# Performance work log

Measured on AMD Instinct MI355X. Metric: run time of the kernel, lower is better.

Reference implementation:

```python
import jax, jax.numpy as jnp
import numpy as np

C = 1.0          # Poincare ball curvature
EPS = 1e-15      # geoopt-style denominator clamp
ATANH_CLAMP = 1e-7


def _artanh(x):
    x = jnp.clip(x, -1.0 + ATANH_CLAMP, 1.0 - ATANH_CLAMP)
    return 0.5 * (jnp.log1p(x) - jnp.log1p(-x))


def setup_inputs() -> dict:
    key = jax.random.key(0)
    n, d = 8192, 256
    embeddings = jax.random.normal(key, (n, d), dtype=jnp.float32) * 0.01
    return {"embeddings": embeddings}


def reference(embeddings):
    # Pairwise Poincare-ball distance:
    #   dist(x, y) = (2/sqrt(c)) * artanh(sqrt(c) * ||(-x) mobius_add y||)
    # mobius_add(-x, y) = (A*(-x) + B*y) / D with
    #   A = 1 - 2c<x,y> + c||y||^2,  B = 1 - c||x||^2,
    #   D = 1 - 2c<x,y> + c^2 ||x||^2 ||y||^2
    # so ||num||^2 = A^2||x||^2 - 2AB<x,y> + B^2||y||^2, using only Gram-matrix
    # quantities -> avoids the [n,n,d] broadcast the torch code materializes
    # while computing identical math.
    x2 = jnp.sum(embeddings * embeddings, axis=-1)          # [n]
    dot = embeddings @ embeddings.T                          # [n,n]
    xi2 = x2[:, None]                                        # ||x_i||^2
    xj2 = x2[None, :]                                        # ||x_j||^2

    A = 1.0 - 2.0 * C * dot + C * xj2                        # [n,n]
    B = 1.0 - C * xi2                                        # [n,1] broadcast
    D = 1.0 - 2.0 * C * dot + (C * C) * xi2 * xj2            # [n,n]

    num2 = jnp.maximum(A * A * xi2 - 2.0 * A * B * dot + B * B * xj2, 0.0)
    norm = jnp.sqrt(num2) / jnp.maximum(jnp.abs(D), EPS)

    sqrt_c = jnp.sqrt(jnp.asarray(C, embeddings.dtype))
    dists = (2.0 / sqrt_c) * _artanh(sqrt_c * norm)          # [n,n]

    n = embeddings.shape[0]
    probs = jax.nn.sigmoid(-dists) * (1.0 - jnp.eye(n, dtype=dists.dtype))
    return (probs, dists)
```

## Files before the change

### kernel.cpp

```cpp
#include <hip/hip_runtime.h>
#include <hip/hip_bf16.h>
#include <stdint.h>

#define NROW 8192
#define DIM  256
#define TILE 128
#define BK   64

typedef unsigned short u16;
typedef __attribute__((ext_vector_type(8))) short short8;
typedef __attribute__((ext_vector_type(4))) float f32x4;

__device__ __forceinline__ void load_lds16(const void* g, void* l) {
    __builtin_amdgcn_global_load_lds(
        (const __attribute__((address_space(1))) void*)g,
        (__attribute__((address_space(3))) void*)l,
        16, 0, 0);
}

__global__ __launch_bounds__(256) void prep_kernel(const float* __restrict__ emb,
                                                   u16* __restrict__ ebf,
                                                   float* __restrict__ x2) {
    const int row = blockIdx.x;
    const int tid = threadIdx.x;
    float v = emb[(size_t)row * DIM + tid];
    uint32_t bits = __float_as_uint(v);
    uint32_t r = (bits + 0x7FFFu + ((bits >> 16) & 1u)) >> 16;
    ebf[(size_t)row * DIM + tid] = (u16)r;
    float s = v * v;
#pragma unroll
    for (int off = 32; off > 0; off >>= 1) s += __shfl_down(s, off, 64);
    __shared__ float ws4[4];
    if ((tid & 63) == 0) ws4[tid >> 6] = s;
    __syncthreads();
    if (tid == 0) x2[row] = ws4[0] + ws4[1] + ws4[2] + ws4[3];
}

__global__ __launch_bounds__(256, 2) void poincare_kernel(const u16* __restrict__ ebf,
                                                          const float* __restrict__ x2,
                                                          float* __restrict__ out) {
    __shared__ __align__(16) u16 Asm[TILE * BK];
    __shared__ __align__(16) u16 Bsm[TILE * BK];

    const int tid  = threadIdx.x;
    const int wave = tid >> 6;
    const int lane = tid & 63;

    const int brow = blockIdx.x * TILE;
    const int bcol = blockIdx.y * TILE;

    const int wm = (wave & 1) * 64;
    const int wn = (wave >> 1) * 64;

    f32x4 acc[4][4];
#pragma unroll
    for (int m = 0; m < 4; ++m)
#pragma unroll
        for (int n = 0; n < 4; ++n) acc[m][n] = (f32x4){0.f, 0.f, 0.f, 0.f};

    const int srow = lane >> 3;
    const int sc   = (((lane & 7) ^ srow) * 8);

    const int lcol  = lane & 15;
    const int quad  = lane >> 4;
    const int chbase = quad ^ (lane & 7);

    for (int k0 = 0; k0 < DIM; k0 += BK) {
#pragma unroll
        for (int t = 0; t < 4; ++t) {
            const int rr = wave * 32 + t * 8;
            const u16* gA = ebf + (size_t)(brow + rr + srow) * DIM + k0 + sc;
            const u16* gB = ebf + (size_t)(bcol + rr + srow) * DIM + k0 + sc;
            load_lds16(gA, &Asm[rr * BK]);
            load_lds16(gB, &Bsm[rr * BK]);
        }
        __syncthreads();

#pragma unroll
        for (int ks = 0; ks < 2; ++ks) {
            const int cc = chbase ^ (ks << 2);
            short8 af[4], bfr[4];
#pragma unroll
            for (int m = 0; m < 4; ++m) {
                const int row = wm + m * 16 + lcol;
                af[m] = *(const short8*)&Asm[row * BK + cc * 8];
            }
#pragma unroll
            for (int n = 0; n < 4; ++n) {
                const int row = wn + n * 16 + lcol;
                bfr[n] = *(const short8*)&Bsm[row * BK + cc * 8];
            }
#pragma unroll
            for (int m = 0; m < 4; ++m)
#pragma unroll
                for (int n = 0; n < 4; ++n)
                    acc[m][n] = __builtin_amdgcn_mfma_f32_16x16x32_bf16(
                        af[m], bfr[n], acc[m][n], 0, 0, 0);
        }
        __syncthreads();
    }

    float xj2v[4];
#pragma unroll
    for (int n = 0; n < 4; ++n) xj2v[n] = x2[bcol + wn + n * 16 + lcol];

    float* __restrict__ probs = out;
    float* __restrict__ dists = out + (size_t)NROW * NROW;

#pragma unroll
    for (int m = 0; m < 4; ++m) {
#pragma unroll
        for (int r = 0; r < 4; ++r) {
            const int grow = brow + wm + m * 16 + quad * 4 + r;
            const float xi2 = x2[grow];
            const float Bv = 1.f - xi2;
            const size_t rowoff = (size_t)grow * NROW;
#pragma unroll
            for (int n = 0; n < 4; ++n) {
                const int gcol = bcol + wn + n * 16 + lcol;
                const float dot = acc[m][n][r];
                const float xj2 = xj2v[n];
                const float Av = 1.f - 2.f * dot + xj2;
                const float Dv = 1.f - 2.f * dot + xi2 * xj2;
                float num2 = Av * Av * xi2 - 2.f * Av * Bv * dot + Bv * Bv * xj2;
                num2 = fmaxf(num2, 0.f);
                const float den = fmaxf(fabsf(Dv), 1e-15f);
                float t = __builtin_amdgcn_sqrtf(num2) * __builtin_amdgcn_rcpf(den);
                t = fminf(t, 1.f - 1e-7f);
                float dist = __logf((1.f + t) * __builtin_amdgcn_rcpf(1.f - t));
                float prob = 0.5f * (1.f - t);
                if (grow == gcol) { dist = 0.f; prob = 0.f; }
                probs[rowoff + gcol] = prob;
                dists[rowoff + gcol] = dist;
            }
        }
    }
}

extern "C" void kernel_launch(void* const* d_in, const int* in_sizes, int n_in,
                              void* d_out, int out_size, void* d_ws, size_t ws_size,
                              hipStream_t stream) {
    (void)in_sizes; (void)n_in; (void)out_size; (void)ws_size;
    const float* emb = (const float*)d_in[0];
    float* out = (float*)d_out;
    u16*   ebf = (u16*)d_ws;
    float* x2  = (float*)((char*)d_ws + (size_t)NROW * DIM * sizeof(u16));

    prep_kernel<<<NROW, 256, 0, stream>>>(emb, ebf, x2);
    dim3 grid(NROW / TILE, NROW / TILE);
    poincare_kernel<<<grid, 256, 0, stream>>>(ebf, x2, out);
}
```

Before: 547.7 us.

## Transpose MFMA accumulators via lane shuffles for vectorized nontemporal epilogue stores

The epilogue uses a 4x4 in-register transpose built from xor lane shuffles, so each lane holds four consecutive columns of one row. It then writes probs and dists as 16-byte nontemporal vector stores instead of scalar 4-byte stores, and loads xj2 as a float4. The math is rearranged to share one reciprocal per element, and the occupancy hint is raised from 2 to 3 blocks. The aim is to cut store instruction count and cache pollution on the 512 MB output write, at the cost of extra shuffle work and more register pressure.

```diff
diff --git a/kernel.cpp b/kernel.cpp
--- a/kernel.cpp
+++ b/kernel.cpp
@@ -36,7 +36,7 @@
     if (tid == 0) x2[row] = ws4[0] + ws4[1] + ws4[2] + ws4[3];
 }
 
-__global__ __launch_bounds__(256, 2) void poincare_kernel(const u16* __restrict__ ebf,
+__global__ __launch_bounds__(256, 3) void poincare_kernel(const u16* __restrict__ ebf,
                                                           const float* __restrict__ x2,
                                                           float* __restrict__ out) {
     __shared__ __align__(16) u16 Asm[TILE * BK];
@@ -100,39 +100,68 @@
         __syncthreads();
     }
 
-    float xj2v[4];
-#pragma unroll
-    for (int n = 0; n < 4; ++n) xj2v[n] = x2[bcol + wn + n * 16 + lcol];
+    const int j4 = lane & 3;
+    const int c4 = lane & 12;
 
     float* __restrict__ probs = out;
     float* __restrict__ dists = out + (size_t)NROW * NROW;
 
 #pragma unroll
     for (int m = 0; m < 4; ++m) {
+        const int grow = brow + wm + m * 16 + quad * 4 + j4;
+        const float xi2 = x2[grow];
+        const float Bv  = 1.f - xi2;
+        const float Bv2 = Bv * Bv;
+        const size_t rowoff = (size_t)grow * NROW;
 #pragma unroll
-        for (int r = 0; r < 4; ++r) {
-            const int grow = brow + wm + m * 16 + quad * 4 + r;
-            const float xi2 = x2[grow];
-            const float Bv = 1.f - xi2;
-            const size_t rowoff = (size_t)grow * NROW;
+        for (int n = 0; n < 4; ++n) {
+            float v0 = acc[m][n][0], v1 = acc[m][n][1],
+                  v2 = acc[m][n][2], v3 = acc[m][n][3];
+            const bool s1 = (j4 & 1) != 0;
+            float a0 = __shfl_xor(v1, 1);
+            float a1 = __shfl_xor(v0, 1);
+            float a2 = __shfl_xor(v3, 1);
+            float a3 = __shfl_xor(v2, 1);
+            float u0 = s1 ? a0 : v0;
+            float u1 = s1 ? v1 : a1;
+            float u2 = s1 ? a2 : v2;
+            float u3 = s1 ? v3 : a3;
+            const bool s2 = (j4 & 2) != 0;
+            float b0 = __shfl_xor(u2, 2);
+            float b1 = __shfl_xor(u3, 2);
+            float b2 = __shfl_xor(u0, 2);
+            float b3 = __shfl_xor(u1, 2);
+            float w0 = s2 ? b0 : u0;
+            float w1 = s2 ? b1 : u1;
+            float w2 = s2 ? u2 : b2;
+            float w3 = s2 ? u3 : b3;
+            float w[4] = {w0, w1, w2, w3};
+
+            const int gcolbase = bcol + wn + n * 16 + c4;
+            const f32x4 xj2v = *(const f32x4*)&x2[gcolbase];
+            f32x4 pr, dv;
 #pragma unroll
-            for (int n = 0; n < 4; ++n) {
-                const int gcol = bcol + wn + n * 16 + lcol;
-                const float dot = acc[m][n][r];
-                const float xj2 = xj2v[n];
+            for (int r = 0; r < 4; ++r) {
+                const float dot = w[r];
+                const float xj2 = xj2v[r];
                 const float Av = 1.f - 2.f * dot + xj2;
                 const float Dv = 1.f - 2.f * dot + xi2 * xj2;
-                float num2 = Av * Av * xi2 - 2.f * Av * Bv * dot + Bv * Bv * xj2;
+                float num2 = Av * Av * xi2 - 2.f * Av * Bv * dot + Bv2 * xj2;
                 num2 = fmaxf(num2, 0.f);
                 const float den = fmaxf(fabsf(Dv), 1e-15f);
-                float t = __builtin_amdgcn_sqrtf(num2) * __builtin_amdgcn_rcpf(den);
-                t = fminf(t, 1.f - 1e-7f);
-                float dist = __logf((1.f + t) * __builtin_amdgcn_rcpf(1.f - t));
-                float prob = 0.5f * (1.f - t);
-                if (grow == gcol) { dist = 0.f; prob = 0.f; }
-                probs[rowoff + gcol] = prob;
-                dists[rowoff + gcol] = dist;
+                float s = __builtin_amdgcn_sqrtf(num2);
+                s = fminf(s, den * 0.9999999f);
+                const float dm = den - s;
+                const float R  = __builtin_amdgcn_rcpf(den * dm);
+                const float t  = s * dm * R;
+                float dist = __logf((den + s) * den * R);
+                float prob = fmaf(-0.5f, t, 0.5f);
+                if (grow == gcolbase + r) { dist = 0.f; prob = 0.f; }
+                pr[r] = prob;
+                dv[r] = dist;
             }
+            __builtin_nontemporal_store(pr, (f32x4*)(probs + rowoff + gcolbase));
+            __builtin_nontemporal_store(dv, (f32x4*)(dists + rowoff + gcolbase));
         }
     }
 }
```

Result: slower. 617.9 us (+12.8%).
